# Kernel optimization log

Hardware: AMD Instinct MI355X
Metric: run time of the kernel (lower is better)

The kernel has to match this reference:

```python
import jax, jax.numpy as jnp
import numpy as np

SCALE = 8      # scale_factor from map_to_mat_info
PATCH = 32     # up_delta - low_delta + 1 == right_delta - left_delta + 1 (uniform interior patches)


def setup_inputs() -> dict:
    key = jax.random.key(0)
    mat_h, mat_w = 160, 160
    H = (mat_h - 1) * SCALE + PATCH  # 1304: deltas (0,31,0,31) -> no border clipping
    W = (mat_w - 1) * SCALE + PATCH
    x = jax.random.normal(key, (1, 3, H, W), dtype=jnp.float32)
    rgb_weight = jnp.array([0.299, 0.587, 0.114], dtype=jnp.float32).reshape(1, 3, 1, 1)
    return {"x": x, "rgb_weight": rgb_weight, "mat_h": mat_h, "mat_w": mat_w}


def reference(x, rgb_weight, mat_h, mat_w):
    P = PATCH
    # RGB -> grayscale (convert_gray branch for in_channels == 3)
    gray = jnp.sum(x * rgb_weight, axis=1)[0]  # (H, W)
    # Gather all overlapping PxP patches at stride SCALE -> (mat_h, mat_w, P, P)
    rows = (jnp.arange(mat_h) * SCALE)[:, None] + jnp.arange(P)[None, :]  # (mat_h, P)
    cols = (jnp.arange(mat_w) * SCALE)[:, None] + jnp.arange(P)[None, :]  # (mat_w, P)
    p = gray[rows.reshape(-1)].reshape(mat_h, P, -1)              # (mat_h, P, W)
    p = p[:, :, cols.reshape(-1)].reshape(mat_h, P, mat_w, P)     # (mat_h, P, mat_w, P)
    patches = jnp.transpose(p, (0, 2, 1, 3))                      # (mat_h, mat_w, P, P)
    # torch.rfft(signal_ndim=2, onesided=False) == full 2D FFT; power = re^2 + im^2
    F = jnp.fft.fft2(patches)
    log_power = jnp.log(F.real * F.real + F.imag * F.imag + 1.0)
    # High-frequency region sums (h == w == P, static)
    lo = P // 2 - P // 4 - 1   # 7
    up = P // 2 + P // 4       # 24
    r1 = jnp.sum(log_power[..., lo:up + 1, :], axis=(-2, -1))
    r2 = jnp.sum(log_power[..., up + 1:, lo:up + 1], axis=(-2, -1))
    r3 = jnp.sum(log_power[..., :lo, lo:up + 1], axis=(-2, -1))
    mat = (r1 + r2 + r3)[None, None]  # (1, 1, mat_h, mat_w)
    return mat / jnp.max(mat)
```

## Files before the change

kernel.cpp:

```cpp
#include <hip/hip_runtime.h>
#include <math.h>

#define SCALE 8
#define PSZ 32

__device__ constexpr float C32[16] = {
     1.000000000000000f,  0.980785280403230f,  0.923879532511287f,  0.831469612302545f,
     0.707106781186548f,  0.555570233019602f,  0.382683432365090f,  0.195090322016128f,
     0.000000000000000f, -0.195090322016128f, -0.382683432365090f, -0.555570233019602f,
    -0.707106781186548f, -0.831469612302545f, -0.923879532511287f, -0.980785280403230f };
__device__ constexpr float S32[16] = {
     0.000000000000000f,  0.195090322016128f,  0.382683432365090f,  0.555570233019602f,
     0.707106781186548f,  0.831469612302545f,  0.923879532511287f,  0.980785280403230f,
     1.000000000000000f,  0.980785280403230f,  0.923879532511287f,  0.831469612302545f,
     0.707106781186548f,  0.555570233019602f,  0.382683432365090f,  0.195090322016128f };

__device__ __forceinline__ constexpr int brev4(int i) {
    return ((i & 1) << 3) | ((i & 2) << 1) | ((i & 4) >> 1) | ((i & 8) >> 3);
}

__device__ __forceinline__ void fft16(float re[16], float im[16]) {
#pragma unroll
    for (int i = 0; i < 16; ++i) {
        const int j = brev4(i);
        if (j > i) {
            float t = re[i]; re[i] = re[j]; re[j] = t;
            t = im[i]; im[i] = im[j]; im[j] = t;
        }
    }
#pragma unroll
    for (int s = 1; s <= 4; ++s) {
        const int m = 1 << s;
        const int h = m >> 1;
        const int tstep = 32 >> s;
#pragma unroll
        for (int k = 0; k < 16; k += m) {
#pragma unroll
            for (int j = 0; j < h; ++j) {
                const float wr = C32[j * tstep];
                const float wi = -S32[j * tstep];
                const int a = k + j;
                const int b = k + j + h;
                const float tr = wr * re[b] - wi * im[b];
                const float ti = wr * im[b] + wi * re[b];
                re[b] = re[a] - tr; im[b] = im[a] - ti;
                re[a] = re[a] + tr; im[a] = im[a] + ti;
            }
        }
    }
}

__device__ __forceinline__ unsigned pack_bf2(float hi, float lo) {
    const unsigned uh = __float_as_uint(hi) + 0x8000u;
    const unsigned ul = __float_as_uint(lo) + 0x8000u;
    return (uh & 0xFFFF0000u) | (ul >> 16);
}
__device__ __forceinline__ float bf_hi(unsigned u) { return __uint_as_float(u & 0xFFFF0000u); }
__device__ __forceinline__ float bf_lo(unsigned u) { return __uint_as_float(u << 16); }

__global__ __launch_bounds__(256) void gray_kernel(
        const float* __restrict__ x, const float* __restrict__ w,
        float* __restrict__ g, int n4, long long HW) {
    const int i = blockIdx.x * 256 + threadIdx.x;
    if (i >= n4) return;
    const float w0 = w[0], w1 = w[1], w2 = w[2];
    const float4 a = reinterpret_cast<const float4*>(x)[i];
    const float4 b = reinterpret_cast<const float4*>(x + HW)[i];
    const float4 c = reinterpret_cast<const float4*>(x + 2 * HW)[i];
    float4 o;
    o.x = w0 * a.x + w1 * b.x + w2 * c.x;
    o.y = w0 * a.y + w1 * b.y + w2 * c.y;
    o.z = w0 * a.z + w1 * b.z + w2 * c.z;
    o.w = w0 * a.w + w1 * b.w + w2 * c.w;
    reinterpret_cast<float4*>(g)[i] = o;
}

__global__ __launch_bounds__(256) void hfdft_tile_kernel(
        const float* __restrict__ g, float* __restrict__ out,
        int W, int mat_w) {
    __shared__ unsigned spec[2 * 88 * 17];

    const int tid = threadIdx.x;
    const int row0 = blockIdx.y * 64;
    const int col0 = blockIdx.x * 16;

    if (tid < 88) {
        const int y = tid;
        const float4* g4 = reinterpret_cast<const float4*>(
            g + (size_t)(row0 + y) * W + col0);
        unsigned* sA = spec + y * 17;
        unsigned* sB = spec + 88 * 17 + y * 17;

        {
            float win[40];
#pragma unroll
            for (int q = 0; q < 10; ++q) {
                const float4 v = g4[q];
                win[4 * q + 0] = v.x; win[4 * q + 1] = v.y;
                win[4 * q + 2] = v.z; win[4 * q + 3] = v.w;
            }
            float er[16], ei[16];
#pragma unroll
            for (int i = 0; i < 16; ++i) {
                er[i] = win[i] + win[i + 16];
                ei[i] = win[i + 8] + win[i + 24];
            }
            fft16(er, ei);
            sA[0] = pack_bf2(er[0], er[8]);
            sB[0] = pack_bf2(ei[0], ei[8]);
#pragma unroll
            for (int k2 = 1; k2 <= 7; ++k2) {
                const int e2 = 16 - k2;
                const float far_ = 0.5f * (er[k2] + er[e2]);
                const float fai_ = 0.5f * (ei[k2] - ei[e2]);
                const float fbr_ = 0.5f * (ei[k2] + ei[e2]);
                const float fbi_ = 0.5f * (er[e2] - er[k2]);
                sA[2 * k2] = pack_bf2(far_, fai_);
                sB[2 * k2] = pack_bf2(fbr_, fbi_);
            }
        }

        asm volatile("" ::: "memory");

        {
            float win[40];
#pragma unroll
            for (int q = 0; q < 10; ++q) {
                const float4 v = g4[q];
                win[4 * q + 0] = v.x; win[4 * q + 1] = v.y;
                win[4 * q + 2] = v.z; win[4 * q + 3] = v.w;
            }
            float orr[16], oi[16];
#pragma unroll
            for (int i = 0; i < 16; ++i) {
                const float dre = win[i] - win[i + 16];
                const float dim = win[i + 8] - win[i + 24];
                orr[i] = dre * C32[i] + dim * S32[i];
                oi[i]  = dim * C32[i] - dre * S32[i];
            }
            fft16(orr, oi);
#pragma unroll
            for (int k2 = 0; k2 <= 7; ++k2) {
                const int o2 = 15 - k2;
                const float far_ = 0.5f * (orr[k2] + orr[o2]);
                const float fai_ = 0.5f * (oi[k2] - oi[o2]);
                const float fbr_ = 0.5f * (oi[k2] + oi[o2]);
                const float fbi_ = 0.5f * (orr[o2] - orr[k2]);
                sA[2 * k2 + 1] = pack_bf2(far_, fai_);
                sB[2 * k2 + 1] = pack_bf2(fbr_, fbi_);
            }
        }
    }

    __syncthreads();

    {
        const int pl = tid >> 4;
        const int slot = tid & 15;
        const int ph = pl >> 1, strip = pl & 1;
        const unsigned* cbp = spec + strip * (88 * 17) + (ph * 8) * 17 + slot;
        const float b1f = (slot >= 7) ? 1.0f : 0.0f;
        const float m1f = (slot >= 8) ? 1.0f : 0.0f;

        float s0 = 0.0f, s1 = 0.0f;

        {
            float er[16], ei[16];
#pragma unroll
            for (int i = 0; i < 16; ++i) {
                const unsigned u0 = cbp[i * 17], u1 = cbp[(i + 16) * 17];
                er[i] = bf_hi(u0) + bf_hi(u1);
                ei[i] = bf_lo(u0) + bf_lo(u1);
            }
            fft16(er, ei);
            if (slot == 0) {
#pragma unroll
                for (int k2 = 0; k2 <= 8; ++k2) {
                    const int kr = 2 * k2;
                    const int b = (k2 == 0) ? 0 : 16 - k2;
                    const float g0r = 0.5f * (er[k2] + er[b]);
                    const float g0i = 0.5f * (ei[k2] - ei[b]);
                    const float g1r = 0.5f * (ei[k2] + ei[b]);
                    const float g1i = 0.5f * (er[b] - er[k2]);
                    const float w0c = (kr >= 7 ? 1.0f : 0.0f) + ((kr >= 8 && kr <= 15) ? 1.0f : 0.0f);
                    const float w16c = 1.0f + ((kr >= 1 && kr <= 15) ? 1.0f : 0.0f);
                    if (w0c > 0.0f)
                        s0 = fmaf(w0c, __logf(g0r * g0r + g0i * g0i + 1.0f), s0);
                    s1 = fmaf(w16c, __logf(g1r * g1r + g1i * g1i + 1.0f), s1);
                }
            } else {
#pragma unroll
                for (int k2 = 0; k2 < 16; ++k2) {
                    const int kr = 2 * k2;
                    const float lp = __logf(er[k2] * er[k2] + ei[k2] * ei[k2] + 1.0f);
                    const float wgt = (kr >= 8 && kr <= 24) ? 2.0f : (b1f + m1f);
                    if (k2 & 1) s1 = fmaf(wgt, lp, s1);
                    else        s0 = fmaf(wgt, lp, s0);
                }
            }
        }

        asm volatile("" ::: "memory");

        {
            float orr[16], oi[16];
#pragma unroll
            for (int i = 0; i < 16; ++i) {
                const unsigned u0 = cbp[i * 17], u1 = cbp[(i + 16) * 17];
                const float dre = bf_hi(u0) - bf_hi(u1);
                const float dim = bf_lo(u0) - bf_lo(u1);
                orr[i] = dre * C32[i] + dim * S32[i];
                oi[i]  = dim * C32[i] - dre * S32[i];
            }
            fft16(orr, oi);
            if (slot == 0) {
#pragma unroll
                for (int k2 = 0; k2 <= 7; ++k2) {
                    const int kr = 2 * k2 + 1;
                    const int b = 15 - k2;
                    const float g0r = 0.5f * (orr[k2] + orr[b]);
                    const float g0i = 0.5f * (oi[k2] - oi[b]);
                    const float g1r = 0.5f * (oi[k2] + oi[b]);
                    const float g1i = 0.5f * (orr[b] - orr[k2]);
                    const float w0c = (kr >= 7 ? 1.0f : 0.0f) + ((kr >= 8 && kr <= 15) ? 1.0f : 0.0f);
                    const float w16c = 2.0f;
                    if (w0c > 0.0f)
                        s0 = fmaf(w0c, __logf(g0r * g0r + g0i * g0i + 1.0f), s0);
                    s1 = fmaf(w16c, __logf(g1r * g1r + g1i * g1i + 1.0f), s1);
                }
            } else {
#pragma unroll
                for (int k2 = 0; k2 < 16; ++k2) {
                    const int kr = 2 * k2 + 1;
                    const float lp = __logf(orr[k2] * orr[k2] + oi[k2] * oi[k2] + 1.0f);
                    float wgt;
                    if (kr == 7)                   wgt = 1.0f + m1f;
                    else if (kr == 25)             wgt = b1f + 1.0f;
                    else if (kr >= 9 && kr <= 23)  wgt = 2.0f;
                    else                           wgt = b1f + m1f;
                    if (k2 & 1) s1 = fmaf(wgt, lp, s1);
                    else        s0 = fmaf(wgt, lp, s0);
                }
            }
        }

        float s = s0 + s1;
#pragma unroll
        for (int off = 8; off >= 1; off >>= 1) s += __shfl_xor(s, off, 16);
        if (slot == 0)
            out[(blockIdx.y * 8 + ph) * mat_w + blockIdx.x * 2 + strip] = s;
    }
}

template <bool GRAY_PRE>
__global__ __launch_bounds__(128) void hfdft_patch_kernel(
        const float* __restrict__ x, const float* __restrict__ w,
        float* __restrict__ out, int H, int W, int mat_h, int mat_w) {
    __shared__ unsigned cb[4 * 528];
    __shared__ float red[8];

    const int tid = threadIdx.x;
    const int h = tid >> 6;
    const int lane = tid & 63;
    const int total = mat_h * mat_w;
    const long long HW = (long long)H * W;
    const int Pbase = blockIdx.x * 4;

    {
        const int g = lane >> 5, r = lane & 31;
        int pA = Pbase + 2 * g;
        if (pA > total - 1) pA = total - 1;
        int pB = pA + 1; if (pB > total - 1) pB = total - 1;
        const int phA = pA / mat_w, pwA = pA % mat_w;
        const int phB = pB / mat_w, pwB = pB % mat_w;
        const bool adj = (phA == phB) && (pwB == pwA + 1);
        const int baseA = (phA * SCALE + r) * W + pwA * SCALE;
        const int baseB = (phB * SCALE + r) * W + pwB * SCALE;

        float ar[32], br[32];
        if (GRAY_PRE && adj) {
            float win[40];
            const float4* g4 = reinterpret_cast<const float4*>(x + baseA);
#pragma unroll
            for (int q = 0; q < 10; ++q) {
                const float4 v = g4[q];
                win[4 * q + 0] = v.x; win[4 * q + 1] = v.y;
                win[4 * q + 2] = v.z; win[4 * q + 3] = v.w;
            }
#pragma unroll
            for (int i = 0; i < 32; ++i) { ar[i] = win[i]; br[i] = win[i + 8]; }
        } else if (GRAY_PRE) {
#pragma unroll
            for (int i = 0; i < 32; ++i) { ar[i] = x[baseA + i]; br[i] = x[baseB + i]; }
        } else {
            const float w0 = w[0], w1 = w[1], w2 = w[2];
#pragma unroll
            for (int i = 0; i < 32; ++i) {
                ar[i] = w0 * x[baseA + i] + w1 * x[HW + baseA + i] + w2 * x[2 * HW + baseA + i];
                br[i] = w0 * x[baseB + i] + w1 * x[HW + baseB + i] + w2 * x[2 * HW + baseB + i];
            }
        }

        float fr[16], fi[16];
        if (h == 0) {
#pragma unroll
            for (int i = 0; i < 16; ++i) {
                fr[i] = ar[i] + ar[i + 16];
                fi[i] = br[i] + br[i + 16];
            }
        } else {
#pragma unroll
            for (int i = 0; i < 16; ++i) {
                const float dre = ar[i] - ar[i + 16];
                const float dim = br[i] - br[i + 16];
                fr[i] = dre * C32[i] + dim * S32[i];
                fi[i] = dim * C32[i] - dre * S32[i];
            }
        }

        fft16(fr, fi);

        unsigned* cbA = cb + (2 * g) * 528;
        unsigned* cbB = cbA + 528;
        if (h == 0) {
            cbA[r] = pack_bf2(fr[0], fr[8]);
            cbB[r] = pack_bf2(fi[0], fi[8]);
#pragma unroll
            for (int k2 = 1; k2 <= 7; ++k2) {
                const int e2 = 16 - k2;
                const float far_ = 0.5f * (fr[k2] + fr[e2]);
                const float fai_ = 0.5f * (fi[k2] - fi[e2]);
                const float fbr_ = 0.5f * (fi[k2] + fi[e2]);
                const float fbi_ = 0.5f * (fr[e2] - fr[k2]);
                cbA[(2 * k2) * 33 + r] = pack_bf2(far_, fai_);
                cbB[(2 * k2) * 33 + r] = pack_bf2(fbr_, fbi_);
            }
        } else {
#pragma unroll
            for (int k2 = 0; k2 <= 7; ++k2) {
                const int o2 = 15 - k2;
                const float far_ = 0.5f * (fr[k2] + fr[o2]);
                const float fai_ = 0.5f * (fi[k2] - fi[o2]);
                const float fbr_ = 0.5f * (fi[k2] + fi[o2]);
                const float fbi_ = 0.5f * (fr[o2] - fr[k2]);
                cbA[(2 * k2 + 1) * 33 + r] = pack_bf2(far_, fai_);
                cbB[(2 * k2 + 1) * 33 + r] = pack_bf2(fbr_, fbi_);
            }
        }
    }

    __syncthreads();

    {
        const int pl = lane >> 4, slot = lane & 15;
        int p = Pbase + pl;
        if (p > total - 1) p = total - 1;
        const unsigned* cbp = cb + pl * 528 + slot * 33;

        float fr[16], fi[16];
        if (h == 0) {
#pragma unroll
            for (int i = 0; i < 16; ++i) {
                const unsigned u0 = cbp[i], u1 = cbp[i + 16];
                fr[i] = bf_hi(u0) + bf_hi(u1);
                fi[i] = bf_lo(u0) + bf_lo(u1);
            }
        } else {
#pragma unroll
            for (int i = 0; i < 16; ++i) {
                const unsigned u0 = cbp[i], u1 = cbp[i + 16];
                const float dre = bf_hi(u0) - bf_hi(u1);
                const float dim = bf_lo(u0) - bf_lo(u1);
                fr[i] = dre * C32[i] + dim * S32[i];
                fi[i] = dim * C32[i] - dre * S32[i];
            }
        }

        fft16(fr, fi);

        float s0 = 0.0f, s1 = 0.0f;
        if (slot == 0) {
            if (h == 0) {
#pragma unroll
                for (int k2 = 0; k2 <= 8; ++k2) {
                    const int kr = 2 * k2;
                    const int b = (k2 == 0) ? 0 : 16 - k2;
                    const float g0r = 0.5f * (fr[k2] + fr[b]);
                    const float g0i = 0.5f * (fi[k2] - fi[b]);
                    const float g1r = 0.5f * (fi[k2] + fi[b]);
                    const float g1i = 0.5f * (fr[b] - fr[k2]);
                    const float w0c = (kr >= 7 ? 1.0f : 0.0f) + ((kr >= 8 && kr <= 15) ? 1.0f : 0.0f);
                    const float w16c = 1.0f + ((kr >= 1 && kr <= 15) ? 1.0f : 0.0f);
                    if (w0c > 0.0f)
                        s0 = fmaf(w0c, __logf(g0r * g0r + g0i * g0i + 1.0f), s0);
                    s1 = fmaf(w16c, __logf(g1r * g1r + g1i * g1i + 1.0f), s1);
                }
            } else {
#pragma unroll
                for (int k2 = 0; k2 <= 7; ++k2) {
                    const int kr = 2 * k2 + 1;
                    const int b = 15 - k2;
                    const float g0r = 0.5f * (fr[k2] + fr[b]);
                    const float g0i = 0.5f * (fi[k2] - fi[b]);
                    const float g1r = 0.5f * (fi[k2] + fi[b]);
                    const float g1i = 0.5f * (fr[b] - fr[k2]);
                    const float w0c = (kr >= 7 ? 1.0f : 0.0f) + ((kr >= 8 && kr <= 15) ? 1.0f : 0.0f);
                    const float w16c = 2.0f;
                    if (w0c > 0.0f)
                        s0 = fmaf(w0c, __logf(g0r * g0r + g0i * g0i + 1.0f), s0);
                    s1 = fmaf(w16c, __logf(g1r * g1r + g1i * g1i + 1.0f), s1);
                }
            }
        } else {
            const float b1f = (slot >= 7) ? 1.0f : 0.0f;
            const float m1f = (slot >= 8) ? 1.0f : 0.0f;
            if (h == 0) {
#pragma unroll
                for (int k2 = 0; k2 < 16; ++k2) {
                    const int kr = 2 * k2;
                    const float lp = __logf(fr[k2] * fr[k2] + fi[k2] * fi[k2] + 1.0f);
                    const float wgt = (kr >= 8 && kr <= 24) ? 2.0f : (b1f + m1f);
                    if (k2 & 1) s1 = fmaf(wgt, lp, s1);
                    else        s0 = fmaf(wgt, lp, s0);
                }
            } else {
#pragma unroll
                for (int k2 = 0; k2 < 16; ++k2) {
                    const int kr = 2 * k2 + 1;
                    const float lp = __logf(fr[k2] * fr[k2] + fi[k2] * fi[k2] + 1.0f);
                    float wgt;
                    if (kr == 7)                   wgt = 1.0f + m1f;
                    else if (kr == 25)             wgt = b1f + 1.0f;
                    else if (kr >= 9 && kr <= 23)  wgt = 2.0f;
                    else                           wgt = b1f + m1f;
                    if (k2 & 1) s1 = fmaf(wgt, lp, s1);
                    else        s0 = fmaf(wgt, lp, s0);
                }
            }
        }

        float s = s0 + s1;
#pragma unroll
        for (int off = 8; off >= 1; off >>= 1) s += __shfl_xor(s, off, 16);
        if (slot == 0) red[pl * 2 + h] = s;
    }

    __syncthreads();

    if (tid < 4) {
        const int p = Pbase + tid;
        if (p < total) out[p] = red[tid * 2] + red[tid * 2 + 1];
    }
}

__global__ __launch_bounds__(1024) void max_kernel(
        const float* __restrict__ sums, int n, float* __restrict__ partial) {
    __shared__ float sm[16];
    float m = 0.0f;
    for (int i = blockIdx.x * 1024 + threadIdx.x; i < n; i += gridDim.x * 1024)
        m = fmaxf(m, sums[i]);
#pragma unroll
    for (int off = 32; off >= 1; off >>= 1) m = fmaxf(m, __shfl_xor(m, off, 64));
    if ((threadIdx.x & 63) == 0) sm[threadIdx.x >> 6] = m;
    __syncthreads();
    if (threadIdx.x == 0) {
#pragma unroll
        for (int i = 1; i < 16; ++i) m = fmaxf(m, sm[i]);
        partial[blockIdx.x] = m;
    }
}

__global__ __launch_bounds__(256) void norm_kernel(
        float* __restrict__ out, int n, const float* __restrict__ partial) {
    const int i = blockIdx.x * 256 + threadIdx.x;
    float m = partial[0];
#pragma unroll
    for (int b = 1; b < 8; ++b) m = fmaxf(m, partial[b]);
    if (i < n) out[i] = out[i] / m;
}

extern "C" void kernel_launch(void* const* d_in, const int* in_sizes, int n_in,
                              void* d_out, int out_size, void* d_ws, size_t ws_size,
                              hipStream_t stream) {
    const float* x = (const float*)d_in[0];
    const float* w = (const float*)d_in[1];
    float* out = (float*)d_out;

    const int HWi = in_sizes[0] / 3;
    const int H = (int)(sqrt((double)HWi) + 0.5);
    const int W = H;
    const long long HW = (long long)H * W;
    const int mat = (int)(sqrt((double)out_size) + 0.5);
    const int total = mat * mat;

    float* partial = (float*)d_ws;
    float* gray = (float*)((char*)d_ws + 256);
    const size_t need = 256 + (size_t)HW * 4;

    const bool shape_ok = ((mat & 7) == 0) && (W == (mat - 1) * SCALE + PSZ)
                          && (H == W) && ((W & 3) == 0);

    if (shape_ok && ws_size >= need) {
        const int n4 = (int)(HW / 4);
        hipLaunchKernelGGL(gray_kernel, dim3((n4 + 255) / 256), dim3(256), 0, stream,
                           x, w, gray, n4, HW);
        dim3 gridT(mat / 2, mat / 8);
        hipLaunchKernelGGL(hfdft_tile_kernel, gridT, dim3(256), 0, stream,
                           gray, out, W, mat);
    } else if (ws_size >= need && (W & 3) == 0) {
        const int n4 = (int)(HW / 4);
        hipLaunchKernelGGL(gray_kernel, dim3((n4 + 255) / 256), dim3(256), 0, stream,
                           x, w, gray, n4, HW);
        hipLaunchKernelGGL((hfdft_patch_kernel<true>), dim3((total + 3) / 4), dim3(128), 0, stream,
                           gray, w, out, H, W, mat, mat);
    } else {
        hipLaunchKernelGGL((hfdft_patch_kernel<false>), dim3((total + 3) / 4), dim3(128), 0, stream,
                           x, w, out, H, W, mat, mat);
    }
    hipLaunchKernelGGL(max_kernel, dim3(8), dim3(1024), 0, stream, out, total, partial);
    hipLaunchKernelGGL(norm_kernel, dim3((total + 255) / 256), dim3(256), 0, stream,
                       out, total, partial);
}
```

Baseline: 43.65 us.

## Fuse grayscale into tile kernel, split even/odd rows across threads, fuse max

```diff
diff --git a/kernel.cpp b/kernel.cpp
--- a/kernel.cpp
+++ b/kernel.cpp
@@ -76,76 +76,75 @@
 }
 
 __global__ __launch_bounds__(256) void hfdft_tile_kernel(
-        const float* __restrict__ g, float* __restrict__ out,
-        int W, int mat_w) {
+        const float* __restrict__ x, const float* __restrict__ w,
+        float* __restrict__ out, float* __restrict__ partial,
+        int W, int mat_w, long long HW) {
     __shared__ unsigned spec[2 * 88 * 17];
+    __shared__ float red[16];
 
     const int tid = threadIdx.x;
     const int row0 = blockIdx.y * 64;
     const int col0 = blockIdx.x * 16;
 
-    if (tid < 88) {
-        const int y = tid;
-        const float4* g4 = reinterpret_cast<const float4*>(
-            g + (size_t)(row0 + y) * W + col0);
+    const bool is_even = (tid < 88);
+    const bool is_odd = (tid >= 128 && tid < 216);
+    if (is_even || is_odd) {
+        const int y = is_even ? tid : (tid - 128);
+        const float* base = x + (size_t)(row0 + y) * W + col0;
+        const float4* a4 = reinterpret_cast<const float4*>(base);
+        const float4* b4 = reinterpret_cast<const float4*>(base + HW);
+        const float4* c4 = reinterpret_cast<const float4*>(base + 2 * HW);
+        const float w0 = w[0], w1 = w[1], w2 = w[2];
+
+        float win[40];
+#pragma unroll
+        for (int q = 0; q < 10; ++q) {
+            const float4 a = a4[q], b = b4[q], c = c4[q];
+            win[4 * q + 0] = w0 * a.x + w1 * b.x + w2 * c.x;
+            win[4 * q + 1] = w0 * a.y + w1 * b.y + w2 * c.y;
+            win[4 * q + 2] = w0 * a.z + w1 * b.z + w2 * c.z;
+            win[4 * q + 3] = w0 * a.w + w1 * b.w + w2 * c.w;
+        }
+
         unsigned* sA = spec + y * 17;
         unsigned* sB = spec + 88 * 17 + y * 17;
 
-        {
-            float win[40];
-#pragma unroll
-            for (int q = 0; q < 10; ++q) {
-                const float4 v = g4[q];
-                win[4 * q + 0] = v.x; win[4 * q + 1] = v.y;
-                win[4 * q + 2] = v.z; win[4 * q + 3] = v.w;
-            }
-            float er[16], ei[16];
-#pragma unroll
-            for (int i = 0; i < 16; ++i) {
-                er[i] = win[i] + win[i + 16];
-                ei[i] = win[i + 8] + win[i + 24];
-            }
-            fft16(er, ei);
-            sA[0] = pack_bf2(er[0], er[8]);
-            sB[0] = pack_bf2(ei[0], ei[8]);
+        float fr[16], fi[16];
+        if (is_even) {
+#pragma unroll
+            for (int i = 0; i < 16; ++i) {
+                fr[i] = win[i] + win[i + 16];
+                fi[i] = win[i + 8] + win[i + 24];
+            }
+            fft16(fr, fi);
+            sA[0] = pack_bf2(fr[0], fr[8]);
+            sB[0] = pack_bf2(fi[0], fi[8]);
 #pragma unroll
             for (int k2 = 1; k2 <= 7; ++k2) {
                 const int e2 = 16 - k2;
-                const float far_ = 0.5f * (er[k2] + er[e2]);
-                const float fai_ = 0.5f * (ei[k2] - ei[e2]);
-                const float fbr_ = 0.5f * (ei[k2] + ei[e2]);
-                const float fbi_ = 0.5f * (er[e2] - er[k2]);
+                const float far_ = 0.5f * (fr[k2] + fr[e2]);
+                const float fai_ = 0.5f * (fi[k2] - fi[e2]);
+                const float fbr_ = 0.5f * (fi[k2] + fi[e2]);
+                const float fbi_ = 0.5f * (fr[e2] - fr[k2]);
                 sA[2 * k2] = pack_bf2(far_, fai_);
                 sB[2 * k2] = pack_bf2(fbr_, fbi_);
             }
-        }
-
-        asm volatile("" ::: "memory");
-
-        {
-            float win[40];
-#pragma unroll
-            for (int q = 0; q < 10; ++q) {
-                const float4 v = g4[q];
-                win[4 * q + 0] = v.x; win[4 * q + 1] = v.y;
-                win[4 * q + 2] = v.z; win[4 * q + 3] = v.w;
-            }
-            float orr[16], oi[16];
+        } else {
 #pragma unroll
             for (int i = 0; i < 16; ++i) {
                 const float dre = win[i] - win[i + 16];
                 const float dim = win[i + 8] - win[i + 24];
-                orr[i] = dre * C32[i] + dim * S32[i];
-                oi[i]  = dim * C32[i] - dre * S32[i];
-            }
-            fft16(orr, oi);
+                fr[i] = dre * C32[i] + dim * S32[i];
+                fi[i] = dim * C32[i] - dre * S32[i];
+            }
+            fft16(fr, fi);
 #pragma unroll
             for (int k2 = 0; k2 <= 7; ++k2) {
                 const int o2 = 15 - k2;
-                const float far_ = 0.5f * (orr[k2] + orr[o2]);
-                const float fai_ = 0.5f * (oi[k2] - oi[o2]);
-                const float fbr_ = 0.5f * (oi[k2] + oi[o2]);
-                const float fbi_ = 0.5f * (orr[o2] - orr[k2]);
+                const float far_ = 0.5f * (fr[k2] + fr[o2]);
+                const float fai_ = 0.5f * (fi[k2] - fi[o2]);
+                const float fbr_ = 0.5f * (fi[k2] + fi[o2]);
+                const float fbi_ = 0.5f * (fr[o2] - fr[k2]);
                 sA[2 * k2 + 1] = pack_bf2(far_, fai_);
                 sB[2 * k2 + 1] = pack_bf2(fbr_, fbi_);
             }
@@ -247,8 +246,19 @@
         float s = s0 + s1;
 #pragma unroll
         for (int off = 8; off >= 1; off >>= 1) s += __shfl_xor(s, off, 16);
-        if (slot == 0)
+        if (slot == 0) {
             out[(blockIdx.y * 8 + ph) * mat_w + blockIdx.x * 2 + strip] = s;
+            red[pl] = s;
+        }
+    }
+
+    __syncthreads();
+
+    if (tid == 0) {
+        float m = red[0];
+#pragma unroll
+        for (int i = 1; i < 16; ++i) m = fmaxf(m, red[i]);
+        partial[blockIdx.y * gridDim.x + blockIdx.x] = m;
     }
 }
 
@@ -471,11 +481,17 @@
 }
 
 __global__ __launch_bounds__(256) void norm_kernel(
-        float* __restrict__ out, int n, const float* __restrict__ partial) {
+        float* __restrict__ out, int n,
+        const float* __restrict__ partial, int np) {
+    __shared__ float sm[4];
+    float m = 0.0f;
+    for (int i = threadIdx.x; i < np; i += 256) m = fmaxf(m, partial[i]);
+#pragma unroll
+    for (int off = 32; off >= 1; off >>= 1) m = fmaxf(m, __shfl_xor(m, off, 64));
+    if ((threadIdx.x & 63) == 0) sm[threadIdx.x >> 6] = m;
+    __syncthreads();
+    m = fmaxf(fmaxf(sm[0], sm[1]), fmaxf(sm[2], sm[3]));
     const int i = blockIdx.x * 256 + threadIdx.x;
-    float m = partial[0];
-#pragma unroll
-    for (int b = 1; b < 8; ++b) m = fmaxf(m, partial[b]);
     if (i < n) out[i] = out[i] / m;
 }
 
@@ -494,30 +510,33 @@
     const int total = mat * mat;
 
     float* partial = (float*)d_ws;
-    float* gray = (float*)((char*)d_ws + 256);
-    const size_t need = 256 + (size_t)HW * 4;
+    float* gray = (float*)((char*)d_ws + 8192);
+    const int nparts = (mat / 2) * (mat / 8);
 
     const bool shape_ok = ((mat & 7) == 0) && (W == (mat - 1) * SCALE + PSZ)
-                          && (H == W) && ((W & 3) == 0);
-
-    if (shape_ok && ws_size >= need) {
-        const int n4 = (int)(HW / 4);
-        hipLaunchKernelGGL(gray_kernel, dim3((n4 + 255) / 256), dim3(256), 0, stream,
-                           x, w, gray, n4, HW);
+                          && (H == W) && ((W & 3) == 0)
+                          && ws_size >= (size_t)nparts * 4;
+
+    if (shape_ok) {
         dim3 gridT(mat / 2, mat / 8);
         hipLaunchKernelGGL(hfdft_tile_kernel, gridT, dim3(256), 0, stream,
-                           gray, out, W, mat);
-    } else if (ws_size >= need && (W & 3) == 0) {
+                           x, w, out, partial, W, mat, HW);
+        hipLaunchKernelGGL(norm_kernel, dim3((total + 255) / 256), dim3(256), 0, stream,
+                           out, total, partial, nparts);
+    } else if (ws_size >= 8192 + (size_t)HW * 4 && (W & 3) == 0) {
         const int n4 = (int)(HW / 4);
         hipLaunchKernelGGL(gray_kernel, dim3((n4 + 255) / 256), dim3(256), 0, stream,
                            x, w, gray, n4, HW);
         hipLaunchKernelGGL((hfdft_patch_kernel<true>), dim3((total + 3) / 4), dim3(128), 0, stream,
                            gray, w, out, H, W, mat, mat);
+        hipLaunchKernelGGL(max_kernel, dim3(8), dim3(1024), 0, stream, out, total, partial);
+        hipLaunchKernelGGL(norm_kernel, dim3((total + 255) / 256), dim3(256), 0, stream,
+                           out, total, partial, 8);
     } else {
         hipLaunchKernelGGL((hfdft_patch_kernel<false>), dim3((total + 3) / 4), dim3(128), 0, stream,
                            x, w, out, H, W, mat, mat);
-    }
-    hipLaunchKernelGGL(max_kernel, dim3(8), dim3(1024), 0, stream, out, total, partial);
-    hipLaunchKernelGGL(norm_kernel, dim3((total + 255) / 256), dim3(256), 0, stream,
-                       out, total, partial);
-}
+        hipLaunchKernelGGL(max_kernel, dim3(8), dim3(1024), 0, stream, out, total, partial);
+        hipLaunchKernelGGL(norm_kernel, dim3((total + 255) / 256), dim3(256), 0, stream,
+                           out, total, partial, 8);
+    }
+}
```

New measurement: 45.01 us. 3.1% more time.
